# Kernel optimization log

Measured on AMD Instinct MI355X. Metric: run time of the kernel, lower is better.

Reference implementation:

```python
import jax, jax.numpy as jnp
import numpy as np

KNN_K = 5  # nearest neighbors for local density
PATCH_GRID = 14  # hard-coded p1=p2=14 in rearrange


def _tokens(x):
    # b c (p1 h) (p2 w) -> b (p1 p2) (h w c)
    B, C, H, W = x.shape
    P = PATCH_GRID
    h, w = H // P, W // P
    t = x.reshape(B, C, P, h, P, w).transpose(0, 2, 4, 3, 5, 1)
    return t.reshape(B, P * P, h * w * C)


def _forward(x, len_keep):
    t = _tokens(x)
    B, N, Cf = t.shape
    # pairwise Euclidean distance (torch.cdist) scaled by sqrt(C)
    sq = jnp.sum(t * t, axis=-1)  # [B, N]
    d2 = sq[:, :, None] + sq[:, None, :] - 2.0 * jnp.einsum('bnc,bmc->bnm', t, t)
    dist = jnp.sqrt(jnp.maximum(d2, 0.0)) / jnp.sqrt(jnp.asarray(Cf, dist_dtype := t.dtype))
    # k-NN local density
    neg_vals, _ = jax.lax.top_k(-dist, KNN_K)  # k smallest distances
    dist_nearest = -neg_vals  # [B, N, k]
    density = jnp.exp(-jnp.mean(dist_nearest ** 2, axis=-1))  # [B, N]
    kd = jax.random.fold_in(jax.random.key(1), 0)
    density = density + jax.random.uniform(kd, density.shape, dtype=density.dtype) * 1e-6
    # distance to nearest higher-density point (masked min reduction)
    maskf = (density[:, None, :] > density[:, :, None]).astype(dist.dtype)  # [B, N, N]
    dist_max = jnp.max(dist.reshape(B, -1), axis=-1)[:, None, None]
    dmin = jnp.min(dist * maskf + dist_max * (1.0 - maskf), axis=-1)  # [B, N]
    score = dmin * density
    # pick cluster centers: top len_keep scores
    _, index_down = jax.lax.top_k(score, len_keep)  # [B, K]
    # assign each token to nearest center
    dm_down = jnp.take_along_axis(dist, index_down[:, :, None], axis=1)  # [B, K, N]
    idx_cluster = jnp.argmin(dm_down, axis=1)  # [B, N]
    # force centers to their own cluster id
    idx_cluster = idx_cluster.at[jnp.arange(B)[:, None], index_down].set(
        jnp.arange(len_keep)[None, :])
    # per-cluster counts (every cluster id 0..K-1 present since centers self-assign)
    counts = jnp.sum(jax.nn.one_hot(idx_cluster, len_keep, dtype=jnp.int32), axis=1)  # [B, K]
    idx_counts = jnp.cumsum(counts, axis=-1)
    # pick one representative token per cluster via noisy sort
    kn = jax.random.fold_in(jax.random.key(1), 1)
    noise = jax.random.uniform(kn, (B, N), dtype=dist.dtype)
    order = jnp.argsort(idx_cluster.astype(dist.dtype) + noise, axis=-1)
    idx = jnp.take_along_axis(order, idx_counts - 1, axis=1)  # [B, K]
    return idx


def setup_inputs() -> dict:
    key = jax.random.key(0)
    x = jax.random.normal(key, (256, 3, 224, 224), dtype=jnp.float32)
    return {"x": x, "len_keep": 49}


def reference(x, len_keep):
    return _forward(x, len_keep)
```

## Files before the change

kernel.cpp:

```cpp
#include <hip/hip_runtime.h>
#include <stdint.h>

#define NTOK 196
#define KCL 49
#define IMG 224
#define IMG2 (224*224)
#define KB 64
#define LDP 68

typedef double f64x4 __attribute__((ext_vector_type(4)));

__host__ __device__ __forceinline__ void tf2x32(uint32_t k0, uint32_t k1,
    uint32_t x0, uint32_t x1, uint32_t* o0, uint32_t* o1) {
  uint32_t ks2 = k0 ^ k1 ^ 0x1BD11BDAu;
#define TFR(r) { x0 += x1; x1 = (x1 << r) | (x1 >> (32 - r)); x1 ^= x0; }
  x0 += k0; x1 += k1;
  TFR(13) TFR(15) TFR(26) TFR(6)
  x0 += k1; x1 += ks2 + 1u;
  TFR(17) TFR(29) TFR(16) TFR(24)
  x0 += ks2; x1 += k0 + 2u;
  TFR(13) TFR(15) TFR(26) TFR(6)
  x0 += k0; x1 += k1 + 3u;
  TFR(17) TFR(29) TFR(16) TFR(24)
  x0 += k1; x1 += ks2 + 4u;
  TFR(13) TFR(15) TFR(26) TFR(6)
  x0 += ks2; x1 += k0 + 5u;
#undef TFR
  *o0 = x0; *o1 = x1;
}

__device__ __forceinline__ float jax_uniform(uint32_t k0, uint32_t k1, uint32_t j) {
  uint32_t o0, o1;
  tf2x32(k0, k1, 0u, j, &o0, &o1);
  uint32_t bits = o0 ^ o1;
  return __uint_as_float((bits >> 9) | 0x3f800000u) - 1.0f;
}

__global__ void __launch_bounds__(256) k_diag(const float* __restrict__ x,
    double* __restrict__ sq, double* __restrict__ dist,
    unsigned long long* __restrict__ dmax) {
  int bid = blockIdx.x;
  int xcd = bid & 7;
  int s = bid >> 3;
  int b = xcd + 8 * (s / 7);
  int ti = s % 7;
  int n0b = ti * 32;
  int tid = threadIdx.x;

  __shared__ __align__(16) float As0[32][LDP];
  __shared__ __align__(16) float As1[32][LDP];
  __shared__ int rbN[32];
  __shared__ double prsh[3];
  __shared__ int okf;
  __shared__ double sqN[32];

  if (tid < 32) {
    int n = n0b + tid; n = n < NTOK ? n : NTOK - 1;
    rbN[tid] = (n / 14) * 16 * IMG + (n % 14) * 16;
  }
  __syncthreads();

  const float* xb = x + (size_t)b * 3 * IMG2;
  int srow = tid >> 3;
  int sfo  = (tid & 7) * 8;
  int rN = rbN[srow];
  int lane = tid & 63;
  int wid  = tid >> 6;
  int wi = wid >> 1, wj = wid & 1;
  int aq = lane >> 4;
  const float* A0 = &As0[0][0];
  const float* A1 = &As1[0][0];
  int fragA = (wi * 16 + (lane & 15)) * LDP + aq;
  int fragB = (wj * 16 + (lane & 15)) * LDP + aq;

#define LOADD(d0,d1,kc) { int f0 = (kc) + sfo;                               \
    int c_ = f0 >> 8, h_ = (f0 >> 4) & 15, w_ = f0 & 15;                     \
    const float* p_ = xb + c_ * IMG2 + h_ * IMG + w_;                        \
    d0 = *(const float4*)(p_ + rN); d1 = *(const float4*)(p_ + rN + 4); }

  f64x4 acc = {0.0, 0.0, 0.0, 0.0};
  f64x4 acc0 = {0.0, 0.0, 0.0, 0.0};
  float4 ca0, ca1;
  LOADD(ca0, ca1, 0)
  *(float4*)&As0[srow][sfo]     = ca0;
  *(float4*)&As0[srow][sfo + 4] = ca1;
  LOADD(ca0, ca1, KB)
  __syncthreads();

#pragma unroll
  for (int tt = 0; tt < 12; ++tt) {
    const float* cur = (tt & 1) ? A1 : A0;
    float (*nxt)[LDP] = (tt & 1) ? As0 : As1;
    if (tt < 11) {
      *(float4*)&nxt[srow][sfo]     = ca0;
      *(float4*)&nxt[srow][sfo + 4] = ca1;
    }
    if (tt < 10) LOADD(ca0, ca1, (tt + 2) * KB)
#pragma unroll
    for (int k = 0; k < KB; k += 4) {
      double av = (double)cur[fragA + k];
      double bv = (double)cur[fragB + k];
      acc = __builtin_amdgcn_mfma_f64_16x16x4f64(av, bv, acc, 0, 0, 0);
    }
    if (tt == 0) {
      if (wid == 0) {
        double q0 = (double)A0[0 * LDP + lane] * (double)A0[0 * LDP + lane];
        double q1 = (double)A0[1 * LDP + lane] * (double)A0[0 * LDP + lane];
        double q2 = (double)A0[4 * LDP + lane] * (double)A0[0 * LDP + lane];
#pragma unroll
        for (int off = 32; off; off >>= 1) {
          q0 += __shfl_down(q0, off);
          q1 += __shfl_down(q1, off);
          q2 += __shfl_down(q2, off);
        }
        if (lane == 0) { prsh[0] = q0; prsh[1] = q1; prsh[2] = q2; }
      }
      acc0 = acc;
    }
    __syncthreads();
  }
#undef LOADD

  if (tid == 0) {
    double tol = 1e-9 * (1.0 + fabs(prsh[0]));
    int ok0  = fabs(prsh[0] - acc0[0]) <= tol;
    int okP1 = ok0 && (fabs(prsh[1] - acc0[1]) <= tol);
    int okP2 = ok0 && (fabs(prsh[2] - acc0[1]) <= tol);
    okf = okP1 ? 1 : (okP2 ? 2 : 0);
  }
  __syncthreads();
  int mode = okf;

  double (*Dt)[33] = (double(*)[33])A0;

  if (mode) {
#pragma unroll
    for (int i = 0; i < 4; ++i) {
      int lr = (mode == 1) ? (aq * 4 + i) : (aq + 4 * i);
      Dt[wi * 16 + lr][wj * 16 + (lane & 15)] = acc[i];
    }
  } else {
    double s00 = 0, s01 = 0, s10 = 0, s11 = 0;
    int ty2 = tid >> 4, tx2 = tid & 15;
    for (int kc = 0; kc < 768; kc += KB) {
      int f0 = kc + sfo;
      int c_ = f0 >> 8, h_ = (f0 >> 4) & 15, w_ = f0 & 15;
      const float* p_ = xb + c_ * IMG2 + h_ * IMG + w_;
      float4 la0 = *(const float4*)(p_ + rN), la1 = *(const float4*)(p_ + rN + 4);
      __syncthreads();
      *(float4*)&As0[srow][sfo]     = la0;
      *(float4*)&As0[srow][sfo + 4] = la1;
      __syncthreads();
      for (int j = 0; j < KB; ++j) {
        double a0 = (double)As0[ty2][j], a1 = (double)As0[ty2 + 16][j];
        double b0 = (double)As0[tx2][j], b1 = (double)As0[tx2 + 16][j];
        s00 += a0 * b0; s01 += a0 * b1; s10 += a1 * b0; s11 += a1 * b1;
      }
    }
    __syncthreads();
    Dt[ty2][tx2] = s00;       Dt[ty2][tx2 + 16] = s01;
    Dt[ty2 + 16][tx2] = s10;  Dt[ty2 + 16][tx2 + 16] = s11;
  }
  __syncthreads();

  if (tid < 32) {
    double v = Dt[tid][tid];
    sqN[tid] = v;
    int n = n0b + tid;
    if (n < NTOK) sq[b * NTOK + n] = v;
  }
  __syncthreads();

  const double SQ768 = sqrt(768.0);
  int lr2 = tid >> 3, lc0 = (tid & 7) * 4;
  double dv[4];
  double lmax = 0.0;
#pragma unroll
  for (int j = 0; j < 4; ++j) {
    double d2 = sqN[lr2] + sqN[lc0 + j] - 2.0 * Dt[lr2][lc0 + j];
    double d = sqrt(d2 > 0.0 ? d2 : 0.0) / SQ768;
    dv[j] = d;
    lmax = lmax > d ? lmax : d;
  }
  double* red = (double*)A1;
  red[tid] = lmax;
  __syncthreads();
  for (int st = 128; st; st >>= 1) {
    if (tid < st) { double o = red[tid + st]; if (o > red[tid]) red[tid] = o; }
    __syncthreads();
  }
  if (tid == 0) atomicMax(&dmax[b], (unsigned long long)__double_as_longlong(red[0]));

  double* Db = dist + (size_t)b * NTOK * NTOK;
  int n = n0b + lr2, m0 = n0b + lc0;
  if (n < NTOK && m0 < NTOK) {
    if (m0 + 3 < NTOK) {
      f64x4 v = {dv[0], dv[1], dv[2], dv[3]};
      *(f64x4*)(Db + (size_t)n * NTOK + m0) = v;
    } else {
#pragma unroll
      for (int j = 0; j < 4; ++j)
        if (m0 + j < NTOK) Db[(size_t)n * NTOK + m0 + j] = dv[j];
    }
  }
}

__global__ void __launch_bounds__(256) k_offdiag(const float* __restrict__ x,
    const double* __restrict__ sq, double* __restrict__ dist,
    unsigned long long* __restrict__ dmax) {
  int bid = blockIdx.x;
  int xcd = bid & 7;
  int s = bid >> 3;
  int b = xcd + 8 * (s / 21);
  int t = s % 21;
  int ti = 0, rem = t, rl = 6;
  while (rem >= rl) { rem -= rl; rl--; ti++; }
  int tj = ti + 1 + rem;
  int n0b = ti * 32, m0b = tj * 32;
  int tid = threadIdx.x;

  __shared__ __align__(16) float As0[32][LDP];
  __shared__ __align__(16) float As1[32][LDP];
  __shared__ __align__(16) float Bs0[32][LDP];
  __shared__ __align__(16) float Bs1[32][LDP];
  __shared__ int rbN[32], rbM[32];
  __shared__ double prsh[3];
  __shared__ int okf;

  if (tid < 32) {
    int n = n0b + tid; n = n < NTOK ? n : NTOK - 1;
    rbN[tid] = (n / 14) * 16 * IMG + (n % 14) * 16;
  } else if (tid < 64) {
    int m = m0b + (tid - 32); m = m < NTOK ? m : NTOK - 1;
    rbM[tid - 32] = (m / 14) * 16 * IMG + (m % 14) * 16;
  }
  __syncthreads();

  const float* xb = x + (size_t)b * 3 * IMG2;
  int srow = tid >> 3;
  int sfo  = (tid & 7) * 8;
  int rN = rbN[srow], rM = rbM[srow];
  int lane = tid & 63;
  int wid  = tid >> 6;
  int wi = wid >> 1, wj = wid & 1;
  int aq = lane >> 4;
  const float* A0 = &As0[0][0];
  const float* A1 = &As1[0][0];
  const float* B0 = &Bs0[0][0];
  const float* B1 = &Bs1[0][0];
  int fragA = (wi * 16 + (lane & 15)) * LDP + aq;
  int fragB = (wj * 16 + (lane & 15)) * LDP + aq;

#define LOADT(d0,d1,d2,d3,kc) { int f0 = (kc) + sfo;                         \
    int c_ = f0 >> 8, h_ = (f0 >> 4) & 15, w_ = f0 & 15;                     \
    const float* p_ = xb + c_ * IMG2 + h_ * IMG + w_;                        \
    d0 = *(const float4*)(p_ + rN); d1 = *(const float4*)(p_ + rN + 4);      \
    d2 = *(const float4*)(p_ + rM); d3 = *(const float4*)(p_ + rM + 4); }

  f64x4 acc = {0.0, 0.0, 0.0, 0.0};
  f64x4 acc0 = {0.0, 0.0, 0.0, 0.0};
  float4 ca0, ca1, cb0, cb1;
  LOADT(ca0, ca1, cb0, cb1, 0)
  *(float4*)&As0[srow][sfo]     = ca0;
  *(float4*)&As0[srow][sfo + 4] = ca1;
  *(float4*)&Bs0[srow][sfo]     = cb0;
  *(float4*)&Bs0[srow][sfo + 4] = cb1;
  LOADT(ca0, ca1, cb0, cb1, KB)
  __syncthreads();

#pragma unroll
  for (int tt = 0; tt < 12; ++tt) {
    const float* curA = (tt & 1) ? A1 : A0;
    const float* curB = (tt & 1) ? B1 : B0;
    float (*nxtA)[LDP] = (tt & 1) ? As0 : As1;
    float (*nxtB)[LDP] = (tt & 1) ? Bs0 : Bs1;
    if (tt < 11) {
      *(float4*)&nxtA[srow][sfo]     = ca0;
      *(float4*)&nxtA[srow][sfo + 4] = ca1;
      *(float4*)&nxtB[srow][sfo]     = cb0;
      *(float4*)&nxtB[srow][sfo + 4] = cb1;
    }
    if (tt < 10) LOADT(ca0, ca1, cb0, cb1, (tt + 2) * KB)
#pragma unroll
    for (int k = 0; k < KB; k += 4) {
      double av = (double)curA[fragA + k];
      double bv = (double)curB[fragB + k];
      acc = __builtin_amdgcn_mfma_f64_16x16x4f64(av, bv, acc, 0, 0, 0);
    }
    if (tt == 0) {
      if (wid == 0) {
        double q0 = (double)A0[0 * LDP + lane] * (double)B0[0 * LDP + lane];
        double q1 = (double)A0[1 * LDP + lane] * (double)B0[0 * LDP + lane];
        double q2 = (double)A0[4 * LDP + lane] * (double)B0[0 * LDP + lane];
#pragma unroll
        for (int off = 32; off; off >>= 1) {
          q0 += __shfl_down(q0, off);
          q1 += __shfl_down(q1, off);
          q2 += __shfl_down(q2, off);
        }
        if (lane == 0) { prsh[0] = q0; prsh[1] = q1; prsh[2] = q2; }
      }
      acc0 = acc;
    }
    __syncthreads();
  }
#undef LOADT

  if (tid == 0) {
    double tol = 1e-9 * (1.0 + fabs(prsh[0]));
    int ok0  = fabs(prsh[0] - acc0[0]) <= tol;
    int okP1 = ok0 && (fabs(prsh[1] - acc0[1]) <= tol);
    int okP2 = ok0 && (fabs(prsh[2] - acc0[1]) <= tol);
    okf = okP1 ? 1 : (okP2 ? 2 : 0);
  }
  __syncthreads();
  int mode = okf;

  double (*Dt)[33] = (double(*)[33])A0;

  if (mode) {
#pragma unroll
    for (int i = 0; i < 4; ++i) {
      int lr = (mode == 1) ? (aq * 4 + i) : (aq + 4 * i);
      Dt[wi * 16 + lr][wj * 16 + (lane & 15)] = acc[i];
    }
  } else {
    double s00 = 0, s01 = 0, s10 = 0, s11 = 0;
    int ty2 = tid >> 4, tx2 = tid & 15;
    for (int kc = 0; kc < 768; kc += KB) {
      int f0 = kc + sfo;
      int c_ = f0 >> 8, h_ = (f0 >> 4) & 15, w_ = f0 & 15;
      const float* p_ = xb + c_ * IMG2 + h_ * IMG + w_;
      float4 la0 = *(const float4*)(p_ + rN), la1 = *(const float4*)(p_ + rN + 4);
      float4 lb0 = *(const float4*)(p_ + rM), lb1 = *(const float4*)(p_ + rM + 4);
      __syncthreads();
      *(float4*)&As0[srow][sfo]     = la0;
      *(float4*)&As0[srow][sfo + 4] = la1;
      *(float4*)&Bs0[srow][sfo]     = lb0;
      *(float4*)&Bs0[srow][sfo + 4] = lb1;
      __syncthreads();
      for (int j = 0; j < KB; ++j) {
        double a0 = (double)As0[ty2][j], a1 = (double)As0[ty2 + 16][j];
        double b0 = (double)Bs0[tx2][j], b1 = (double)Bs0[tx2 + 16][j];
        s00 += a0 * b0; s01 += a0 * b1; s10 += a1 * b0; s11 += a1 * b1;
      }
    }
    __syncthreads();
    Dt[ty2][tx2] = s00;       Dt[ty2][tx2 + 16] = s01;
    Dt[ty2 + 16][tx2] = s10;  Dt[ty2 + 16][tx2 + 16] = s11;
  }
  __syncthreads();

  const double* sqb = sq + b * NTOK;
  const double SQ768 = sqrt(768.0);
  int lr2 = tid >> 3, lc0 = (tid & 7) * 4;
  double dv[4];
  double lmax = 0.0;
#pragma unroll
  for (int j = 0; j < 4; ++j) {
    int n = n0b + lr2, m = m0b + lc0 + j;
    int nn = n < NTOK ? n : NTOK - 1, mm = m < NTOK ? m : NTOK - 1;
    double d2 = sqb[nn] + sqb[mm] - 2.0 * Dt[lr2][lc0 + j];
    double d = sqrt(d2 > 0.0 ? d2 : 0.0) / SQ768;
    dv[j] = d;
    lmax = lmax > d ? lmax : d;
  }
#pragma unroll
  for (int j = 0; j < 4; ++j) Dt[lr2][lc0 + j] = dv[j];
  double* red = (double*)B0;
  red[tid] = lmax;
  __syncthreads();
  for (int st = 128; st; st >>= 1) {
    if (tid < st) { double o = red[tid + st]; if (o > red[tid]) red[tid] = o; }
    __syncthreads();
  }
  if (tid == 0) atomicMax(&dmax[b], (unsigned long long)__double_as_longlong(red[0]));

  double* Db = dist + (size_t)b * NTOK * NTOK;
  {
    int n = n0b + lr2, m0 = m0b + lc0;
    if (n < NTOK && m0 < NTOK) {
      if (m0 + 3 < NTOK) {
        f64x4 v = {dv[0], dv[1], dv[2], dv[3]};
        *(f64x4*)(Db + (size_t)n * NTOK + m0) = v;
      } else {
#pragma unroll
        for (int j = 0; j < 4; ++j)
          if (m0 + j < NTOK) Db[(size_t)n * NTOK + m0 + j] = dv[j];
      }
    }
  }
  {
    int m = m0b + lr2, n0 = n0b + lc0;
    if (m < NTOK && n0 < NTOK) {
      if (n0 + 3 < NTOK) {
        f64x4 v = {Dt[lc0][lr2], Dt[lc0 + 1][lr2], Dt[lc0 + 2][lr2], Dt[lc0 + 3][lr2]};
        *(f64x4*)(Db + (size_t)m * NTOK + n0) = v;
      } else {
#pragma unroll
        for (int j = 0; j < 4; ++j)
          if (n0 + j < NTOK) Db[(size_t)m * NTOK + n0 + j] = Dt[lc0 + j][lr2];
      }
    }
  }
}

#define INS5(n0_,n1_,n2_,n3_,n4_,v_) {                                        \
  if ((v_) < n4_) { n4_ = (v_);                                               \
    if (n4_ < n3_) { double w_ = n3_; n3_ = n4_; n4_ = w_;                    \
      if (n3_ < n2_) { w_ = n2_; n2_ = n3_; n3_ = w_;                         \
        if (n2_ < n1_) { w_ = n1_; n1_ = n2_; n2_ = w_;                       \
          if (n1_ < n0_) { w_ = n0_; n0_ = n1_; n1_ = w_; } } } } } }

__global__ void __launch_bounds__(512) k_cluster2(const double* __restrict__ dist,
    const unsigned long long* __restrict__ dmax, int* __restrict__ out,
    uint32_t kd0, uint32_t kd1, uint32_t kn0, uint32_t kn1, int B) {
  int b = blockIdx.x;
  int tid = threadIdx.x;
  int lane = tid & 63, wid = tid >> 6;
  const double* Db = dist + (size_t)b * NTOK * NTOK;
  __shared__ double nbsh[NTOK * 5];
  __shared__ double dens[NTOK];
  __shared__ double score[NTOK];
  __shared__ int center[KCL];
  __shared__ short center_of[NTOK];
  __shared__ unsigned long long bkey[KCL];
  double dmaxv = __longlong_as_double((long long)dmax[b]);

  int t = (tid < NTOK) ? tid : tid - NTOK;
  int half = (tid < NTOK) ? 0 : 1;
  bool act = tid < 2 * NTOK;
  int m0 = half ? 98 : 0;

  double pa0 = 1e300, pa1 = 1e300, pa2 = 1e300, pa3 = 1e300, pa4 = 1e300;
  double qa0 = 1e300, qa1 = 1e300, qa2 = 1e300, qa3 = 1e300, qa4 = 1e300;
  if (act) {
    const double* base = Db + t;
    for (int i = 0; i < 49; ++i) {
      double v1 = base[(size_t)(m0 + i) * NTOK];
      double v2 = base[(size_t)(m0 + 49 + i) * NTOK];
      INS5(pa0, pa1, pa2, pa3, pa4, v1)
      INS5(qa0, qa1, qa2, qa3, qa4, v2)
    }
  }
  double nb[5];
  {
    double ax = pa0, a1 = pa1, a2 = pa2, a3 = pa3, a4 = pa4;
    double bx = qa0, b1 = qa1, b2 = qa2, b3 = qa3, b4 = qa4;
#pragma unroll
    for (int p = 0; p < 5; ++p) {
      if (ax <= bx) { nb[p] = ax; ax = a1; a1 = a2; a2 = a3; a3 = a4; a4 = 1e300; }
      else          { nb[p] = bx; bx = b1; b1 = b2; b2 = b3; b3 = b4; b4 = 1e300; }
    }
  }
  if (act && half) {
    nbsh[t * 5 + 0] = nb[0]; nbsh[t * 5 + 1] = nb[1]; nbsh[t * 5 + 2] = nb[2];
    nbsh[t * 5 + 3] = nb[3]; nbsh[t * 5 + 4] = nb[4];
  }
  __syncthreads();
  if (tid < NTOK) {
    double ax = nb[0], a1 = nb[1], a2 = nb[2], a3 = nb[3], a4 = nb[4];
    double bx = nbsh[t * 5 + 0], b1 = nbsh[t * 5 + 1], b2 = nbsh[t * 5 + 2],
           b3 = nbsh[t * 5 + 3], b4 = nbsh[t * 5 + 4];
    double acc = 0.0;
#pragma unroll
    for (int p = 0; p < 5; ++p) {
      double v;
      if (ax <= bx) { v = ax; ax = a1; a1 = a2; a2 = a3; a3 = a4; a4 = 1e300; }
      else          { v = bx; bx = b1; b1 = b2; b2 = b3; b3 = b4; b4 = 1e300; }
      acc += v * v;
    }
    double d = exp(-(acc / 5.0));
    double u = (double)jax_uniform(kd0, kd1, (uint32_t)(b * NTOK + t));
    dens[t] = d + u * 1e-6;
  }
  __syncthreads();

  double vloc = dmaxv;
  if (act) {
    double dn = dens[t];
    const double* base = Db + t;
    double v1 = dmaxv, v2 = dmaxv;
    for (int i = 0; i < 49; ++i) {
      double r1 = base[(size_t)(m0 + i) * NTOK];
      double r2 = base[(size_t)(m0 + 49 + i) * NTOK];
      if (dens[m0 + i] > dn && r1 < v1) v1 = r1;
      if (dens[m0 + 49 + i] > dn && r2 < v2) v2 = r2;
    }
    vloc = v1 < v2 ? v1 : v2;
  }
  __syncthreads();
  if (act && half) nbsh[t] = vloc;
  __syncthreads();
  if (tid < NTOK) {
    double v2 = nbsh[t];
    double v = vloc < v2 ? vloc : v2;
    score[t] = v * dens[t];
  }
  __syncthreads();

  if (wid == 0) {
    double s0 = (lane < NTOK) ? score[lane] : -1e300;
    double s1 = score[lane + 64];
    double s2 = score[lane + 128];
    double s3 = (lane + 192 < NTOK) ? score[lane + 192] : -1e300;
    for (int k = 0; k < KCL; ++k) {
      double mv = s0; int mi = lane;
      if (s1 > mv) { mv = s1; mi = lane + 64; }
      if (s2 > mv) { mv = s2; mi = lane + 128; }
      if (s3 > mv) { mv = s3; mi = lane + 192; }
#pragma unroll
      for (int off = 32; off; off >>= 1) {
        double ov = __shfl_down(mv, off); int oi = __shfl_down(mi, off);
        if (ov > mv || (ov == mv && oi < mi)) { mv = ov; mi = oi; }
      }
      mi = __shfl(mi, 0);
      if (lane == 0) center[k] = mi;
      if (mi == lane) s0 = -1e300;
      else if (mi == lane + 64) s1 = -1e300;
      else if (mi == lane + 128) s2 = -1e300;
      else if (mi == lane + 192) s3 = -1e300;
    }
  }
  __syncthreads();

  if (tid < NTOK) center_of[tid] = -1;
  __syncthreads();
  if (tid < KCL) { center_of[center[tid]] = (short)tid; bkey[tid] = 0ULL; }
  __syncthreads();
  int mycl = 0;
  if (tid < NTOK) {
    double best = 1e300; int bk = 0;
    for (int k = 0; k < KCL; ++k) {
      double d = Db[(size_t)center[k] * NTOK + tid];
      if (d < best) { best = d; bk = k; }
    }
    short co = center_of[tid];
    if (co >= 0) bk = co;
    mycl = bk;
  }
  __syncthreads();

  if (tid < NTOK) {
    float u = jax_uniform(kn0, kn1, (uint32_t)(b * NTOK + tid));
    float keyf = (float)mycl + u;
    unsigned long long key =
        ((unsigned long long)__float_as_uint(keyf) << 8) | (unsigned)tid;
    atomicMax(&bkey[mycl], key);
  }
  __syncthreads();
  if (tid < KCL) out[b * KCL + tid] = (int)(bkey[tid] & 0xFFu);
}

extern "C" void kernel_launch(void* const* d_in, const int* in_sizes, int n_in,
                              void* d_out, int out_size, void* d_ws, size_t ws_size,
                              hipStream_t stream) {
  const float* x = (const float*)d_in[0];
  int B = in_sizes[0] / (3 * IMG2);
  double* dist = (double*)d_ws;
  size_t distBytes = (size_t)B * NTOK * NTOK * sizeof(double);
  double* sq = (double*)((char*)d_ws + distBytes);
  unsigned long long* dmax =
      (unsigned long long*)((char*)sq + (size_t)B * NTOK * sizeof(double));
  int* out = (int*)d_out;

  uint32_t kd0, kd1, kn0, kn1;
  tf2x32(0u, 1u, 0u, 0u, &kd0, &kd1);
  tf2x32(0u, 1u, 0u, 1u, &kn0, &kn1);

  hipMemsetAsync(dmax, 0, B * sizeof(unsigned long long), stream);
  k_diag<<<dim3(8 * 32 * 7), dim3(256), 0, stream>>>(x, sq, dist, dmax);
  k_offdiag<<<dim3(8 * 32 * 21), dim3(256), 0, stream>>>(x, sq, dist, dmax);
  k_cluster2<<<dim3(B), dim3(512), 0, stream>>>(dist, dmax, out, kd0, kd1, kn0, kn1, B);
}
```

Baseline: 303.3 us.

## Single-buffer LDS in GEMM kernels and split cluster kernel columns four ways

The diag and off-diag distance kernels drop double-buffered shared memory and switch to a single buffer: the next tile is prefetched into registers and two barriers guard each store. This cuts LDS use per block, which may raise occupancy, but adds a barrier per iteration and less overlap. The cluster kernel moves from 512 to 1024 threads, splitting each token's column scan into four 49-row chunks. The partial top-5 lists and masked minima are merged through shared memory, giving more memory-level parallelism on a grid of only B blocks.

```diff
diff --git a/kernel.cpp b/kernel.cpp
--- a/kernel.cpp
+++ b/kernel.cpp
@@ -47,12 +47,12 @@
   int n0b = ti * 32;
   int tid = threadIdx.x;
 
-  __shared__ __align__(16) float As0[32][LDP];
-  __shared__ __align__(16) float As1[32][LDP];
+  __shared__ __align__(16) float As[32][LDP];
   __shared__ int rbN[32];
   __shared__ double prsh[3];
   __shared__ int okf;
   __shared__ double sqN[32];
+  __shared__ double red2[256];
 
   if (tid < 32) {
     int n = n0b + tid; n = n < NTOK ? n : NTOK - 1;
@@ -68,8 +68,7 @@
   int wid  = tid >> 6;
   int wi = wid >> 1, wj = wid & 1;
   int aq = lane >> 4;
-  const float* A0 = &As0[0][0];
-  const float* A1 = &As1[0][0];
+  const float* A0 = &As[0][0];
   int fragA = (wi * 16 + (lane & 15)) * LDP + aq;
   int fragB = (wj * 16 + (lane & 15)) * LDP + aq;
 
@@ -82,31 +81,26 @@
   f64x4 acc0 = {0.0, 0.0, 0.0, 0.0};
   float4 ca0, ca1;
   LOADD(ca0, ca1, 0)
-  *(float4*)&As0[srow][sfo]     = ca0;
-  *(float4*)&As0[srow][sfo + 4] = ca1;
-  LOADD(ca0, ca1, KB)
-  __syncthreads();
 
 #pragma unroll
   for (int tt = 0; tt < 12; ++tt) {
-    const float* cur = (tt & 1) ? A1 : A0;
-    float (*nxt)[LDP] = (tt & 1) ? As0 : As1;
-    if (tt < 11) {
-      *(float4*)&nxt[srow][sfo]     = ca0;
-      *(float4*)&nxt[srow][sfo + 4] = ca1;
-    }
-    if (tt < 10) LOADD(ca0, ca1, (tt + 2) * KB)
+    __syncthreads();
+    *(float4*)&As[srow][sfo]     = ca0;
+    *(float4*)&As[srow][sfo + 4] = ca1;
+    __syncthreads();
+    float4 na0, na1;
+    if (tt < 11) LOADD(na0, na1, (tt + 1) * KB)
 #pragma unroll
     for (int k = 0; k < KB; k += 4) {
-      double av = (double)cur[fragA + k];
-      double bv = (double)cur[fragB + k];
+      double av = (double)A0[fragA + k];
+      double bv = (double)A0[fragB + k];
       acc = __builtin_amdgcn_mfma_f64_16x16x4f64(av, bv, acc, 0, 0, 0);
     }
     if (tt == 0) {
       if (wid == 0) {
-        double q0 = (double)A0[0 * LDP + lane] * (double)A0[0 * LDP + lane];
-        double q1 = (double)A0[1 * LDP + lane] * (double)A0[0 * LDP + lane];
-        double q2 = (double)A0[4 * LDP + lane] * (double)A0[0 * LDP + lane];
+        double q0 = (double)As[0][lane] * (double)As[0][lane];
+        double q1 = (double)As[1][lane] * (double)As[0][lane];
+        double q2 = (double)As[4][lane] * (double)As[0][lane];
 #pragma unroll
         for (int off = 32; off; off >>= 1) {
           q0 += __shfl_down(q0, off);
@@ -117,7 +111,7 @@
       }
       acc0 = acc;
     }
-    __syncthreads();
+    ca0 = na0; ca1 = na1;
   }
 #undef LOADD
 
@@ -148,12 +142,12 @@
       const float* p_ = xb + c_ * IMG2 + h_ * IMG + w_;
       float4 la0 = *(const float4*)(p_ + rN), la1 = *(const float4*)(p_ + rN + 4);
       __syncthreads();
-      *(float4*)&As0[srow][sfo]     = la0;
-      *(float4*)&As0[srow][sfo + 4] = la1;
+      *(float4*)&As[srow][sfo]     = la0;
+      *(float4*)&As[srow][sfo + 4] = la1;
       __syncthreads();
       for (int j = 0; j < KB; ++j) {
-        double a0 = (double)As0[ty2][j], a1 = (double)As0[ty2 + 16][j];
-        double b0 = (double)As0[tx2][j], b1 = (double)As0[tx2 + 16][j];
+        double a0 = (double)As[ty2][j], a1 = (double)As[ty2 + 16][j];
+        double b0 = (double)As[tx2][j], b1 = (double)As[tx2 + 16][j];
         s00 += a0 * b0; s01 += a0 * b1; s10 += a1 * b0; s11 += a1 * b1;
       }
     }
@@ -182,14 +176,13 @@
     dv[j] = d;
     lmax = lmax > d ? lmax : d;
   }
-  double* red = (double*)A1;
-  red[tid] = lmax;
+  red2[tid] = lmax;
   __syncthreads();
   for (int st = 128; st; st >>= 1) {
-    if (tid < st) { double o = red[tid + st]; if (o > red[tid]) red[tid] = o; }
-    __syncthreads();
-  }
-  if (tid == 0) atomicMax(&dmax[b], (unsigned long long)__double_as_longlong(red[0]));
+    if (tid < st) { double o = red2[tid + st]; if (o > red2[tid]) red2[tid] = o; }
+    __syncthreads();
+  }
+  if (tid == 0) atomicMax(&dmax[b], (unsigned long long)__double_as_longlong(red2[0]));
 
   double* Db = dist + (size_t)b * NTOK * NTOK;
   int n = n0b + lr2, m0 = n0b + lc0;
@@ -219,10 +212,8 @@
   int n0b = ti * 32, m0b = tj * 32;
   int tid = threadIdx.x;
 
-  __shared__ __align__(16) float As0[32][LDP];
-  __shared__ __align__(16) float As1[32][LDP];
-  __shared__ __align__(16) float Bs0[32][LDP];
-  __shared__ __align__(16) float Bs1[32][LDP];
+  __shared__ __align__(16) float As[32][LDP];
+  __shared__ __align__(16) float Bs[32][LDP];
   __shared__ int rbN[32], rbM[32];
   __shared__ double prsh[3];
   __shared__ int okf;
@@ -244,10 +235,8 @@
   int wid  = tid >> 6;
   int wi = wid >> 1, wj = wid & 1;
   int aq = lane >> 4;
-  const float* A0 = &As0[0][0];
-  const float* A1 = &As1[0][0];
-  const float* B0 = &Bs0[0][0];
-  const float* B1 = &Bs1[0][0];
+  const float* Ap = &As[0][0];
+  const float* Bp = &Bs[0][0];
   int fragA = (wi * 16 + (lane & 15)) * LDP + aq;
   int fragB = (wj * 16 + (lane & 15)) * LDP + aq;
 
@@ -261,37 +250,28 @@
   f64x4 acc0 = {0.0, 0.0, 0.0, 0.0};
   float4 ca0, ca1, cb0, cb1;
   LOADT(ca0, ca1, cb0, cb1, 0)
-  *(float4*)&As0[srow][sfo]     = ca0;
-  *(float4*)&As0[srow][sfo + 4] = ca1;
-  *(float4*)&Bs0[srow][sfo]     = cb0;
-  *(float4*)&Bs0[srow][sfo + 4] = cb1;
-  LOADT(ca0, ca1, cb0, cb1, KB)
-  __syncthreads();
 
 #pragma unroll
   for (int tt = 0; tt < 12; ++tt) {
-    const float* curA = (tt & 1) ? A1 : A0;
-    const float* curB = (tt & 1) ? B1 : B0;
-    float (*nxtA)[LDP] = (tt & 1) ? As0 : As1;
-    float (*nxtB)[LDP] = (tt & 1) ? Bs0 : Bs1;
-    if (tt < 11) {
-      *(float4*)&nxtA[srow][sfo]     = ca0;
-      *(float4*)&nxtA[srow][sfo + 4] = ca1;
-      *(float4*)&nxtB[srow][sfo]     = cb0;
-      *(float4*)&nxtB[srow][sfo + 4] = cb1;
-    }
-    if (tt < 10) LOADT(ca0, ca1, cb0, cb1, (tt + 2) * KB)
+    __syncthreads();
+    *(float4*)&As[srow][sfo]     = ca0;
+    *(float4*)&As[srow][sfo + 4] = ca1;
+    *(float4*)&Bs[srow][sfo]     = cb0;
+    *(float4*)&Bs[srow][sfo + 4] = cb1;
+    __syncthreads();
+    float4 na0, na1, nb0, nb1;
+    if (tt < 11) LOADT(na0, na1, nb0, nb1, (tt + 1) * KB)
 #pragma unroll
     for (int k = 0; k < KB; k += 4) {
-      double av = (double)curA[fragA + k];
-      double bv = (double)curB[fragB + k];
+      double av = (double)Ap[fragA + k];
+      double bv = (double)Bp[fragB + k];
       acc = __builtin_amdgcn_mfma_f64_16x16x4f64(av, bv, acc, 0, 0, 0);
     }
     if (tt == 0) {
       if (wid == 0) {
-        double q0 = (double)A0[0 * LDP + lane] * (double)B0[0 * LDP + lane];
-        double q1 = (double)A0[1 * LDP + lane] * (double)B0[0 * LDP + lane];
-        double q2 = (double)A0[4 * LDP + lane] * (double)B0[0 * LDP + lane];
+        double q0 = (double)As[0][lane] * (double)Bs[0][lane];
+        double q1 = (double)As[1][lane] * (double)Bs[0][lane];
+        double q2 = (double)As[4][lane] * (double)Bs[0][lane];
 #pragma unroll
         for (int off = 32; off; off >>= 1) {
           q0 += __shfl_down(q0, off);
@@ -302,7 +282,7 @@
       }
       acc0 = acc;
     }
-    __syncthreads();
+    ca0 = na0; ca1 = na1; cb0 = nb0; cb1 = nb1;
   }
 #undef LOADT
 
@@ -316,7 +296,7 @@
   __syncthreads();
   int mode = okf;
 
-  double (*Dt)[33] = (double(*)[33])A0;
+  double (*Dt)[33] = (double(*)[33])Ap;
 
   if (mode) {
 #pragma unroll
@@ -334,14 +314,14 @@
       float4 la0 = *(const float4*)(p_ + rN), la1 = *(const float4*)(p_ + rN + 4);
       float4 lb0 = *(const float4*)(p_ + rM), lb1 = *(const float4*)(p_ + rM + 4);
       __syncthreads();
-      *(float4*)&As0[srow][sfo]     = la0;
-      *(float4*)&As0[srow][sfo + 4] = la1;
-      *(float4*)&Bs0[srow][sfo]     = lb0;
-      *(float4*)&Bs0[srow][sfo + 4] = lb1;
+      *(float4*)&As[srow][sfo]     = la0;
+      *(float4*)&As[srow][sfo + 4] = la1;
+      *(float4*)&Bs[srow][sfo]     = lb0;
+      *(float4*)&Bs[srow][sfo + 4] = lb1;
       __syncthreads();
       for (int j = 0; j < KB; ++j) {
-        double a0 = (double)As0[ty2][j], a1 = (double)As0[ty2 + 16][j];
-        double b0 = (double)Bs0[tx2][j], b1 = (double)Bs0[tx2 + 16][j];
+        double a0 = (double)As[ty2][j], a1 = (double)As[ty2 + 16][j];
+        double b0 = (double)Bs[tx2][j], b1 = (double)Bs[tx2 + 16][j];
         s00 += a0 * b0; s01 += a0 * b1; s10 += a1 * b0; s11 += a1 * b1;
       }
     }
@@ -367,7 +347,7 @@
   }
 #pragma unroll
   for (int j = 0; j < 4; ++j) Dt[lr2][lc0 + j] = dv[j];
-  double* red = (double*)B0;
+  double* red = (double*)Bp;
   red[tid] = lmax;
   __syncthreads();
   for (int st = 128; st; st >>= 1) {
@@ -412,14 +392,30 @@
         if (n2_ < n1_) { w_ = n1_; n1_ = n2_; n2_ = w_;                       \
           if (n1_ < n0_) { w_ = n0_; n0_ = n1_; n1_ = w_; } } } } } }
 
-__global__ void __launch_bounds__(512) k_cluster2(const double* __restrict__ dist,
+__device__ __forceinline__ void merge5(double a[5], const double b[5]) {
+  double o[5];
+  double ax = a[0], a1 = a[1], a2 = a[2], a3 = a[3], a4 = a[4];
+  double bx = b[0], b1 = b[1], b2 = b[2], b3 = b[3], b4 = b[4];
+#pragma unroll
+  for (int p = 0; p < 5; ++p) {
+    if (ax <= bx) { o[p] = ax; ax = a1; a1 = a2; a2 = a3; a3 = a4; a4 = 1e300; }
+    else          { o[p] = bx; bx = b1; b1 = b2; b2 = b3; b3 = b4; b4 = 1e300; }
+  }
+#pragma unroll
+  for (int p = 0; p < 5; ++p) a[p] = o[p];
+}
+
+__global__ void __launch_bounds__(1024) k_cluster4(const double* __restrict__ dist,
     const unsigned long long* __restrict__ dmax, int* __restrict__ out,
     uint32_t kd0, uint32_t kd1, uint32_t kn0, uint32_t kn1, int B) {
   int b = blockIdx.x;
   int tid = threadIdx.x;
   int lane = tid & 63, wid = tid >> 6;
+  int t = tid & 255, q = tid >> 8;
+  bool act = t < NTOK;
+  int m0 = q * 49;
   const double* Db = dist + (size_t)b * NTOK * NTOK;
-  __shared__ double nbsh[NTOK * 5];
+  __shared__ double nbsh[2][NTOK][5];
   __shared__ double dens[NTOK];
   __shared__ double score[NTOK];
   __shared__ int center[KCL];
@@ -427,49 +423,42 @@
   __shared__ unsigned long long bkey[KCL];
   double dmaxv = __longlong_as_double((long long)dmax[b]);
 
-  int t = (tid < NTOK) ? tid : tid - NTOK;
-  int half = (tid < NTOK) ? 0 : 1;
-  bool act = tid < 2 * NTOK;
-  int m0 = half ? 98 : 0;
-
-  double pa0 = 1e300, pa1 = 1e300, pa2 = 1e300, pa3 = 1e300, pa4 = 1e300;
-  double qa0 = 1e300, qa1 = 1e300, qa2 = 1e300, qa3 = 1e300, qa4 = 1e300;
+  double nb[5] = {1e300, 1e300, 1e300, 1e300, 1e300};
   if (act) {
     const double* base = Db + t;
     for (int i = 0; i < 49; ++i) {
-      double v1 = base[(size_t)(m0 + i) * NTOK];
-      double v2 = base[(size_t)(m0 + 49 + i) * NTOK];
-      INS5(pa0, pa1, pa2, pa3, pa4, v1)
-      INS5(qa0, qa1, qa2, qa3, qa4, v2)
-    }
-  }
-  double nb[5];
-  {
-    double ax = pa0, a1 = pa1, a2 = pa2, a3 = pa3, a4 = pa4;
-    double bx = qa0, b1 = qa1, b2 = qa2, b3 = qa3, b4 = qa4;
-#pragma unroll
-    for (int p = 0; p < 5; ++p) {
-      if (ax <= bx) { nb[p] = ax; ax = a1; a1 = a2; a2 = a3; a3 = a4; a4 = 1e300; }
-      else          { nb[p] = bx; bx = b1; b1 = b2; b2 = b3; b3 = b4; b4 = 1e300; }
-    }
-  }
-  if (act && half) {
-    nbsh[t * 5 + 0] = nb[0]; nbsh[t * 5 + 1] = nb[1]; nbsh[t * 5 + 2] = nb[2];
-    nbsh[t * 5 + 3] = nb[3]; nbsh[t * 5 + 4] = nb[4];
+      double v = base[(size_t)(m0 + i) * NTOK];
+      INS5(nb[0], nb[1], nb[2], nb[3], nb[4], v)
+    }
+    if (q == 1) {
+#pragma unroll
+      for (int p = 0; p < 5; ++p) nbsh[0][t][p] = nb[p];
+    } else if (q == 3) {
+#pragma unroll
+      for (int p = 0; p < 5; ++p) nbsh[1][t][p] = nb[p];
+    }
+  }
+  __syncthreads();
+  if (act && q == 2) {
+    double ob[5];
+#pragma unroll
+    for (int p = 0; p < 5; ++p) ob[p] = nbsh[1][t][p];
+    merge5(nb, ob);
+#pragma unroll
+    for (int p = 0; p < 5; ++p) nbsh[1][t][p] = nb[p];
   }
   __syncthreads();
   if (tid < NTOK) {
-    double ax = nb[0], a1 = nb[1], a2 = nb[2], a3 = nb[3], a4 = nb[4];
-    double bx = nbsh[t * 5 + 0], b1 = nbsh[t * 5 + 1], b2 = nbsh[t * 5 + 2],
-           b3 = nbsh[t * 5 + 3], b4 = nbsh[t * 5 + 4];
+    double ob[5];
+#pragma unroll
+    for (int p = 0; p < 5; ++p) ob[p] = nbsh[0][t][p];
+    merge5(nb, ob);
+#pragma unroll
+    for (int p = 0; p < 5; ++p) ob[p] = nbsh[1][t][p];
+    merge5(nb, ob);
     double acc = 0.0;
 #pragma unroll
-    for (int p = 0; p < 5; ++p) {
-      double v;
-      if (ax <= bx) { v = ax; ax = a1; a1 = a2; a2 = a3; a3 = a4; a4 = 1e300; }
-      else          { v = bx; bx = b1; b1 = b2; b2 = b3; b3 = b4; b4 = 1e300; }
-      acc += v * v;
-    }
+    for (int p = 0; p < 5; ++p) acc += nb[p] * nb[p];
     double d = exp(-(acc / 5.0));
     double u = (double)jax_uniform(kd0, kd1, (uint32_t)(b * NTOK + t));
     dens[t] = d + u * 1e-6;
@@ -480,21 +469,21 @@
   if (act) {
     double dn = dens[t];
     const double* base = Db + t;
-    double v1 = dmaxv, v2 = dmaxv;
     for (int i = 0; i < 49; ++i) {
-      double r1 = base[(size_t)(m0 + i) * NTOK];
-      double r2 = base[(size_t)(m0 + 49 + i) * NTOK];
-      if (dens[m0 + i] > dn && r1 < v1) v1 = r1;
-      if (dens[m0 + 49 + i] > dn && r2 < v2) v2 = r2;
-    }
-    vloc = v1 < v2 ? v1 : v2;
-  }
-  __syncthreads();
-  if (act && half) nbsh[t] = vloc;
+      double r = base[(size_t)(m0 + i) * NTOK];
+      if (dens[m0 + i] > dn && r < vloc) vloc = r;
+    }
+  }
+  __syncthreads();
+  double* pm = &nbsh[0][0][0];
+  if (act && q > 0) pm[(q - 1) * NTOK + t] = vloc;
   __syncthreads();
   if (tid < NTOK) {
-    double v2 = nbsh[t];
-    double v = vloc < v2 ? vloc : v2;
+    double v = vloc;
+    double p1v = pm[t], p2v = pm[NTOK + t], p3v = pm[2 * NTOK + t];
+    v = p1v < v ? p1v : v;
+    v = p2v < v ? p2v : v;
+    v = p3v < v ? p3v : v;
     score[t] = v * dens[t];
   }
   __syncthreads();
@@ -571,5 +560,5 @@
   hipMemsetAsync(dmax, 0, B * sizeof(unsigned long long), stream);
   k_diag<<<dim3(8 * 32 * 7), dim3(256), 0, stream>>>(x, sq, dist, dmax);
   k_offdiag<<<dim3(8 * 32 * 21), dim3(256), 0, stream>>>(x, sq, dist, dmax);
-  k_cluster2<<<dim3(B), dim3(512), 0, stream>>>(dist, dmax, out, kd0, kd1, kn0, kn1, B);
-}
+  k_cluster4<<<dim3(B), dim3(1024), 0, stream>>>(dist, dmax, out, kd0, kd1, kn0, kn1, B);
+}
```

Result: faster. 293.6 us (-3.2%).
